# Optimization experiments

Measured on AMD Instinct MI355X. Metric: run time of the kernel, lower is better.

## Reference

```python
import jax, jax.numpy as jnp
import numpy as np
from jax import lax

EPS = 1e-5
B, NA, NE, NAL = 1024, 10, 10, 9

def qbn(x):
    # QBN_RM1d: divide by RMS of detached input over all dims but last
    xd = lax.stop_gradient(x)
    mean2 = jnp.mean((xd * xd).reshape(-1, xd.shape[-1]), axis=0)
    return x / jnpp_sqrt(mean2) if False else x / jnp.sqrt(mean2 + EPS)

def qrelu(x):
    # Qrelu1d: scale each 2-vector (axis -2) by mod/max(1,mod), mod from detached x
    xd = lax.stop_gradient(x)
    mod = jnp.sqrt(jnp.sum(xd * xd, axis=-2))
    coeff = mod / jnp.maximum(1.0, mod)
    return x * coeff[..., None, :]

def rcn(x, Ws):
    for W in Ws:
        x = qrelu(qbn(x @ W))
    return x

def qmerge(x):
    return jnp.sum(x * x, axis=-2)

def qmaxpool(x):
    # x: [B,A,N,2,C]; pick per-channel entity with max squared 2-norm
    xd = lax.stop_gradient(x)
    mod = jnp.sum(xd * xd, axis=-2)            # [B,A,N,C]
    idx = jnp.argmax(mod, axis=-2)             # [B,A,C]
    idxb = jnp.broadcast_to(idx[:, :, None, None, :], x.shape[:2] + (1,) + x.shape[-2:])
    return jnp.take_along_axis(x, idxb, axis=-3)[:, :, 0]   # [B,A,2,C]

def build_vec(feats, own_vec):
    # feats: [B,A,n,9]; own_vec: [B,A,2,11]
    pos = feats[..., 2:4][..., None]                          # [B,A,n,2,1]
    pos_mod = jnp.sqrt(jnp.sum(pos * pos, axis=-2))           # [B,A,n,1]
    other = jnp.concatenate([feats[..., :2], feats[..., 4:]], axis=-1)  # [B,A,n,7]
    other_mod = jnp.sqrt(2.0 * other * other)                 # repeat-2 then 2-norm = sqrt(2*x^2)
    mask = pos_mod == 0.0
    denom = jnp.where(mask, 1.0, pos_mod)
    coff = jnp.where(mask, 0.0, other_mod / denom)[..., None, :]   # [B,A,n,1,7]
    vec = pos * coff                                           # [B,A,n,2,7]
    own_mod = jnp.sqrt(jnp.sum(own_vec * own_vec, axis=-2))[:, :, None, :]  # [B,A,1,11]
    own_coff = jnp.where(mask, 0.0, own_mod / denom)[..., None, :]          # [B,A,n,1,11]
    own_vecf = pos * own_coff                                  # [B,A,n,2,11]
    return jnp.concatenate([pos, vec, own_vecf], axis=-1)      # [B,A,n,2,19]

def setup_inputs() -> dict:
    key = jax.random.key(0)
    ks = jax.random.split(key, 32)
    s = 0.1
    inp = {
        'own_feats':   jax.random.normal(ks[0], (B, NA, 11), jnp.float32),
        'enemy_feats': jax.random.normal(ks[1], (B, NA, NE, 9), jnp.float32),
        'ally_feats':  jax.random.normal(ks[2], (B, NA, NAL, 9), jnp.float32),
        'W_e1': jax.random.normal(ks[3], (19, 64), jnp.float32) * s,
        'W_e2': jax.random.normal(ks[4], (64, 64), jnp.float32) * s,
        'W_a1': jax.random.normal(ks[5], (19, 64), jnp.float32) * s,
        'W_a2': jax.random.normal(ks[6], (64, 64), jnp.float32) * s,
        'W_f1': jax.random.normal(ks[7], (64, 64), jnp.float32) * s,
        'W_f2': jax.random.normal(ks[8], (64, 64), jnp.float32) * s,
        'W_ie1': jax.random.normal(ks[9], (128, 64), jnp.float32) * s,
        'W_ie2': jax.random.normal(ks[10], (64, 64), jnp.float32) * s,
        'W_ie3': jax.random.normal(ks[11], (64, 1), jnp.float32) * s,
        'W_ia1': jax.random.normal(ks[12], (128, 64), jnp.float32) * s,
        'W_ia2': jax.random.normal(ks[13], (64, 64), jnp.float32) * s,
        'W_ia3': jax.random.normal(ks[14], (64, 1), jnp.float32) * s,
        'W_oa1': jax.random.normal(ks[15], (64, 64), jnp.float32) * s,
        'b_oa1': jnp.zeros((64,), jnp.float32),
        'W_oa2': jax.random.normal(ks[16], (64, 3), jnp.float32) * s,
        'b_oa2': jnp.zeros((3,), jnp.float32),
        'W_at1': jax.random.normal(ks[17], (128, 128), jnp.float32) * s,
        'b_at1': jnp.zeros((128,), jnp.float32),
        'W_at2': jax.random.normal(ks[18], (128, 64), jnp.float32) * s,
        'b_at2': jnp.zeros((64,), jnp.float32),
        'W_at3': jax.random.normal(ks[19], (64, 1), jnp.float32) * s,
        'b_at3': jnp.zeros((1,), jnp.float32),
    }
    return inp

def reference(own_feats, enemy_feats, ally_feats,
              W_e1, W_e2, W_a1, W_a2, W_f1, W_f2,
              W_ie1, W_ie2, W_ie3, W_ia1, W_ia2, W_ia3,
              W_oa1, b_oa1, W_oa2, b_oa2,
              W_at1, b_at1, W_at2, b_at2, W_at3, b_at3):
    Bc = own_feats.shape[0]
    own_vec = jnp.repeat(own_feats[:, :, None, :], 2, axis=2)        # [B,A,2,11]
    ev = build_vec(enemy_feats, own_vec)                              # [B,A,10,2,19]
    av = build_vec(ally_feats, own_vec)                               # [B,A,9,2,19]
    e_rc = rcn(ev, (W_e1, W_e2))                                      # [B,A,10,2,64]
    e_scalar = qmerge(e_rc)                                           # [B,A,10,64]
    a_rc = rcn(av, (W_a1, W_a2))                                      # [B,A,9,2,64]
    all_rc = jnp.concatenate([e_rc, a_rc], axis=-3)                   # [B,A,19,2,64]
    vf = rcn(qmaxpool(all_rc), (W_f1, W_f2))                          # [B,A,2,64]
    vrep = jnp.broadcast_to(vf[:, :, None], (Bc, NA, NE, 2, 64))
    cat = jnp.concatenate([vrep, e_rc], axis=-1)                      # [B,A,10,2,128]
    e_imp = rcn(cat, (W_ie1, W_ie2, W_ie3))                           # [B,A,10,2,1]
    a_imp = rcn(cat, (W_ia1, W_ia2, W_ia3))                           # (orig code also uses enemy feats here)
    move_vec = jnp.sum(jnp.concatenate([e_imp, a_imp], axis=-3), axis=-3)  # [B,A,2,1]
    sf = qmerge(vf)                                                   # [B,A,64]
    oaq = jax.nn.relu(sf @ W_oa1 + b_oa1) @ W_oa2 + b_oa2             # [B,A,3]
    mmq = oaq[:, :, 2:3]
    up = mmq + move_vec[:, :, 1, :]
    down = mmq - move_vec[:, :, 1, :]
    right = mmq + move_vec[:, :, 0, :]
    left = mmq - move_vec[:, :, 0, :]
    move_q = jnp.concatenate([up, down, right, left], axis=-1)        # [B,A,4]
    sfr = jnp.broadcast_to(sf[:, :, None, :], (Bc, NA, NE, 64))
    atf = jnp.concatenate([sfr, e_scalar], axis=-1)                   # [B,A,10,128]
    h = jax.nn.relu(atf @ W_at1 + b_at1)
    h = jax.nn.relu(h @ W_at2 + b_at2)
    aq = (h @ W_at3 + b_at3)[..., 0]                                  # [B,A,10]
    return jnp.concatenate([oaq[:, :, 0:2], move_q, aq], axis=-1)     # [B,A,16]
```

## Files before the change

### kernel.cpp

```cpp
#include <hip/hip_runtime.h>
#include <math.h>

#define BATCH 1024
#define NA 10
#define NEN 10
#define NALY 9
#define NAG (BATCH*NA)
#define NEE (NAG*NEN)
#define NAE (NAG*NALY)
#define EPSF 1e-5f

#define DOFF_SE1 0
#define DOFF_SE2 1024
#define DOFF_SA1 2048
#define DOFF_SA2 3072
#define DOFF_SF1 4096
#define DOFF_SF2 5120
#define DOFF_SIE1 6144
#define DOFF_SIE2 7168
#define DOFF_SIA1 8192
#define DOFF_SIA2 9216
#define DOFF_SIE3 10240
#define DOFF_SIA3 10368
#define NDOUBLES 16384

#define NBLK_BE (NEE/8)
#define NBLK_BA (NAE/8)
#define NBLK_PE64 (NEE/64)
#define NBLK_PA64 (NAE/64)

__device__ __forceinline__ double sum16vd(const double* __restrict__ S, int ch) {
    double s = 0.0;
#pragma unroll
    for (int r = 0; r < 16; ++r) s += S[r*64 + ch];
    return s;
}
__device__ __forceinline__ double sum16sd8(const double* __restrict__ S) {
    double s = 0.0;
#pragma unroll
    for (int r = 0; r < 16; ++r) s += S[r*8];
    return s;
}
__device__ __forceinline__ float qbn_s(const double* __restrict__ S, int ch, double invRows) {
    float m = (float)(sum16vd(S, ch)*invRows);
    return sqrtf(m + EPSF);
}
__device__ __forceinline__ void red_to_S(const double* red, double* S, int bid, int tid) {
    if (tid < 64) {
        double v = red[tid] + red[tid+64] + red[tid+128] + red[tid+192];
        atomicAdd(&S[(bid & 15)*64 + tid], v);
    }
}
__device__ __forceinline__ float pair_m2(float x0, float x1) {
    return __fadd_rn(__fmul_rn(x0,x0), __fmul_rn(x1,x1));
}
__device__ __forceinline__ float qcoef(float mod) {
    return fminf(mod, 1.0f);
}

__global__ __launch_bounds__(256) void k_build_both(
    const float* __restrict__ ef, const float* __restrict__ af,
    const float* __restrict__ own,
    const float* __restrict__ We1, const float* __restrict__ Wa1,
    float* __restrict__ XE, float* __restrict__ XA,
    double* __restrict__ SE1, double* __restrict__ SA1)
{
    bool isA = (blockIdx.x >= NBLK_BE);
    int blk = isA ? (blockIdx.x - NBLK_BE) : blockIdx.x;
    const float* feats = isA ? af : ef;
    const float* W1    = isA ? Wa1 : We1;
    float* X           = isA ? XA : XE;
    double* S1         = isA ? SA1 : SE1;
    int nEntPerAgent   = isA ? NALY : NEN;

    __shared__ float wlds[19*64];
    __shared__ float gpc[16][19];
    __shared__ double red[256];
    int tid = threadIdx.x;
    for (int i = tid; i < 19*64; i += 256) wlds[i] = W1[i];
    if (tid < 152) {
        int el = tid / 19, chg = tid % 19;
        int ent = blk*8 + el;
        const float* f = feats + (size_t)ent*9;
        int agent = ent / nEntPerAgent;
        float px = f[2], py = f[3];
        float pm = sqrtf(__fadd_rn(__fmul_rn(px,px), __fmul_rn(py,py)));
        float val;
        if (chg == 0) val = 1.f;
        else if (chg < 8) {
            int j = chg - 1;
            int fi = (j < 2) ? j : (j + 2);
            float o = f[fi];
            float om = sqrtf(__fmul_rn(__fmul_rn(2.0f,o),o));
            val = (pm == 0.f) ? 0.f : __fdiv_rn(om, pm);
        } else {
            float o = own[(size_t)agent*11 + (chg-8)];
            float t = __fmul_rn(o,o);
            float om = sqrtf(__fadd_rn(t,t));
            val = (pm == 0.f) ? 0.f : __fdiv_rn(om, pm);
        }
        gpc[el*2 + 0][chg] = __fmul_rn(px, val);
        gpc[el*2 + 1][chg] = __fmul_rn(py, val);
    }
    __syncthreads();
    int l = tid >> 7, c = (tid >> 6) & 1, ch = tid & 63;
    float wreg[19];
#pragma unroll
    for (int k = 0; k < 19; ++k) wreg[k] = wlds[k*64+ch];
    double lr = 0.0;
#pragma unroll
    for (int i = 0; i < 4; ++i) {
        int el = l + 2*i;
        int ent = blk*8 + el;
        int row = el*2 + c;
        float acc = 0.f;
#pragma unroll
        for (int k = 18; k >= 0; --k) {
            acc = fmaf(gpc[row][k], wreg[k], acc);
        }
        X[(size_t)ent*128 + c*64 + ch] = acc;
        lr += (double)acc * (double)acc;
    }
    red[tid] = lr;
    __syncthreads();
    red_to_S(red, S1, blk, tid);
}

__device__ __forceinline__ void pair_layer_body(
    float* __restrict__ X, const double* __restrict__ Sin, double* __restrict__ Sout,
    const float* __restrict__ W, double invRows, int blk)
{
    __shared__ float wlds[4096];
    __shared__ __align__(16) float ybuf[64][132];
    __shared__ float ss[64];
    double* dredw = (double*)&ybuf[0][0];
    int tid = threadIdx.x;
    for (int i = tid; i < 4096; i += 512) wlds[i] = W[i];
    if (tid < 64) ss[tid] = qbn_s(Sin, tid, invRows);
    __syncthreads();
    int rl = tid >> 4;
    int ch0 = (tid & 15) * 4;
#pragma unroll
    for (int h = 0; h < 2; ++h) {
        int r = rl + h*32;
        size_t row = (size_t)blk*64 + r;
        float4 xv0 = *(const float4*)&X[row*128 + ch0];
        float4 xv1 = *(const float4*)&X[row*128 + 64 + ch0];
        float xs0[4] = {xv0.x,xv0.y,xv0.z,xv0.w};
        float xs1[4] = {xv1.x,xv1.y,xv1.z,xv1.w};
        float y0[4], y1[4];
#pragma unroll
        for (int i = 0; i < 4; ++i) {
            float s = ss[ch0+i];
            float u0 = xs0[i]/s, u1 = xs1[i]/s;
            float mod = sqrtf(pair_m2(u0,u1));
            float cf = qcoef(mod);
            y0[i] = __fmul_rn(u0,cf);
            y1[i] = __fmul_rn(u1,cf);
        }
        *(float4*)&ybuf[r][2*ch0]     = make_float4(y0[0],y1[0],y0[1],y1[1]);
        *(float4*)&ybuf[r][2*ch0 + 4] = make_float4(y0[2],y1[2],y0[3],y1[3]);
    }
    __syncthreads();
    float a0[4] = {0.f,0.f,0.f,0.f};
    float a1[4] = {0.f,0.f,0.f,0.f};
    float c0[4] = {0.f,0.f,0.f,0.f};
    float c1[4] = {0.f,0.f,0.f,0.f};
#pragma unroll
    for (int k = 63; k >= 1; k -= 2) {
        float4 wk  = *(const float4*)&wlds[k*64 + ch0];
        float4 wk1 = *(const float4*)&wlds[(k-1)*64 + ch0];
        float4 ya  = *(const float4*)&ybuf[rl][2*k - 2];
        float4 yb  = *(const float4*)&ybuf[rl+32][2*k - 2];
        float wkv[4]  = {wk.x,wk.y,wk.z,wk.w};
        float wk1v[4] = {wk1.x,wk1.y,wk1.z,wk1.w};
#pragma unroll
        for (int i = 0; i < 4; ++i) {
            a0[i] = fmaf(ya.z, wkv[i], a0[i]);
            a1[i] = fmaf(ya.w, wkv[i], a1[i]);
        }
#pragma unroll
        for (int i = 0; i < 4; ++i) {
            a0[i] = fmaf(ya.x, wk1v[i], a0[i]);
            a1[i] = fmaf(ya.y, wk1v[i], a1[i]);
        }
#pragma unroll
        for (int i = 0; i < 4; ++i) {
            c0[i] = fmaf(yb.z, wkv[i], c0[i]);
            c1[i] = fmaf(yb.w, wkv[i], c1[i]);
        }
#pragma unroll
        for (int i = 0; i < 4; ++i) {
            c0[i] = fmaf(yb.x, wk1v[i], c0[i]);
            c1[i] = fmaf(yb.y, wk1v[i], c1[i]);
        }
    }
    size_t rowA = (size_t)blk*64 + rl;
    size_t rowB = rowA + 32;
    *(float4*)&X[rowA*128 + ch0]      = make_float4(a0[0],a0[1],a0[2],a0[3]);
    *(float4*)&X[rowA*128 + 64 + ch0] = make_float4(a1[0],a1[1],a1[2],a1[3]);
    *(float4*)&X[rowB*128 + ch0]      = make_float4(c0[0],c0[1],c0[2],c0[3]);
    *(float4*)&X[rowB*128 + 64 + ch0] = make_float4(c1[0],c1[1],c1[2],c1[3]);
    __syncthreads();
    {
        int wv = tid >> 6;
#pragma unroll
        for (int i = 0; i < 4; ++i) {
            double d = (double)a0[i]*a0[i] + (double)a1[i]*a1[i]
                     + (double)c0[i]*c0[i] + (double)c1[i]*c1[i];
            d += __shfl_xor(d, 16, 64);
            d += __shfl_xor(d, 32, 64);
            if ((tid & 48) == 0) dredw[wv*64 + ch0+i] = d;
        }
    }
    __syncthreads();
    if (tid < 64) {
        double v = 0.0;
#pragma unroll
        for (int w = 0; w < 8; ++w) v += dredw[w*64 + tid];
        atomicAdd(&Sout[(blk & 15)*64 + tid], v);
    }
}

__global__ __launch_bounds__(512) void k_pair_both(
    float* __restrict__ XE, const double* __restrict__ SE1, double* __restrict__ SE2,
    const float* __restrict__ We2, double invRe,
    float* __restrict__ XA, const double* __restrict__ SA1, double* __restrict__ SA2,
    const float* __restrict__ Wa2, double invRa)
{
    if (blockIdx.x < NBLK_PE64)
        pair_layer_body(XE, SE1, SE2, We2, invRe, blockIdx.x);
    else
        pair_layer_body(XA, SA1, SA2, Wa2, invRa, blockIdx.x - NBLK_PE64);
}

__global__ __launch_bounds__(512) void k_pair_layer(
    float* __restrict__ X, const double* __restrict__ Sin, double* __restrict__ Sout,
    const float* __restrict__ W, double invRows)
{
    pair_layer_body(X, Sin, Sout, W, invRows, blockIdx.x);
}

__global__ __launch_bounds__(256) void k_finalize_pair(
    float* __restrict__ X, const double* __restrict__ S2, double invRows,
    float* __restrict__ ESC)
{
    __shared__ float ss[64];
    if (threadIdx.x < 64) ss[threadIdx.x] = qbn_s(S2, threadIdx.x, invRows);
    int t = blockIdx.x*256 + threadIdx.x;
    int rl = t >> 4;
    int ch0 = (t & 15) * 4;
    size_t base    = (size_t)rl*64 + ch0;
    size_t partner = (size_t)(rl ^ 1)*64 + ch0;
    float4 xv  = *(const float4*)&X[base];
    float4 xov = *(const float4*)&X[partner];
    __syncthreads();
    float xs[4]  = {xv.x,xv.y,xv.z,xv.w};
    float xos[4] = {xov.x,xov.y,xov.z,xov.w};
    float r[4], esc[4];
    int c = rl & 1;
#pragma unroll
    for (int i = 0; i < 4; ++i) {
        float s = ss[ch0+i];
        float u  = xs[i]/s;
        float uo = xos[i]/s;
        float u0 = (c==0) ? u : uo, u1 = (c==0) ? uo : u;
        float mod = sqrtf(pair_m2(u0,u1));
        float cf = qcoef(mod);
        r[i] = __fmul_rn(u, cf);
        if (c == 0) {
            float y1v = __fmul_rn(uo, cf);
            esc[i] = pair_m2(r[i], y1v);
        }
    }
    *(float4*)&X[base] = make_float4(r[0],r[1],r[2],r[3]);
    if (c == 0) {
        int ent = rl >> 1;
        *(float4*)&ESC[(size_t)ent*64 + ch0] = make_float4(esc[0],esc[1],esc[2],esc[3]);
    }
}

__global__ __launch_bounds__(256) void k_pool_f1(
    const float* __restrict__ XE, const float* __restrict__ XAraw,
    const double* __restrict__ SA2, double invRa,
    const float* __restrict__ Wf1, float* __restrict__ F1, double* __restrict__ Sf1)
{
    __shared__ float wlds[4096];
    __shared__ float v[4][2][64];
    __shared__ float ssa[64];
    __shared__ double red[256];
    int tid = threadIdx.x;
    for (int i = tid; i < 4096; i += 256) wlds[i] = Wf1[i];
    if (tid < 64) ssa[tid] = qbn_s(SA2, tid, invRa);
    __syncthreads();
    int grp = tid>>6, ch = tid&63;
    int agent = blockIdx.x*4 + grp;
    float best = -1.f, v0 = 0.f, v1 = 0.f;
    for (int e = 0; e < NEN; ++e) {
        size_t b = (size_t)(agent*NEN+e)*128;
        float x0 = XE[b+ch], x1 = XE[b+64+ch];
        float m2 = pair_m2(x0,x1);
        if (m2 > best) { best = m2; v0 = x0; v1 = x1; }
    }
    float sa = ssa[ch];
    for (int l = 0; l < NALY; ++l) {
        size_t b = (size_t)(agent*NALY+l)*128;
        float r0 = XAraw[b+ch], r1 = XAraw[b+64+ch];
        float u0 = r0/sa, u1 = r1/sa;
        float modf = sqrtf(pair_m2(u0,u1));
        float cff = qcoef(modf);
        float x0 = __fmul_rn(u0,cff), x1 = __fmul_rn(u1,cff);
        float m2 = pair_m2(x0,x1);
        if (m2 > best) { best = m2; v0 = x0; v1 = x1; }
    }
    v[grp][0][ch] = v0; v[grp][1][ch] = v1;
    __syncthreads();
    float a0 = 0.f, a1 = 0.f;
#pragma unroll
    for (int k = 0; k < 64; ++k) {
        float w = wlds[k*64+ch];
        a0 = fmaf(v[grp][0][k], w, a0);
        a1 = fmaf(v[grp][1][k], w, a1);
    }
    F1[(size_t)agent*128+ch] = a0; F1[(size_t)agent*128+64+ch] = a1;
    red[tid] = (double)a0*a0 + (double)a1*a1;
    __syncthreads();
    red_to_S(red, Sf1, blockIdx.x, tid);
}

__global__ __launch_bounds__(256) void k_vf_vtop(
    float* __restrict__ F1, const double* __restrict__ Sf2,
    float* __restrict__ SFb,
    const float* __restrict__ Wie1, const float* __restrict__ Wia1,
    const float* __restrict__ Wat1, const float* __restrict__ bat1,
    float* __restrict__ VTie, float* __restrict__ VTia, double invRows)
{
    __shared__ float wie[4096];
    __shared__ float wia[4096];
    __shared__ float vf[4][2][64];
    __shared__ float sfv[4][64];
    int tid = threadIdx.x;
    for (int i = tid; i < 4096; i += 256) { wie[i] = Wie1[i]; wia[i] = Wia1[i]; }
    int grp = tid>>6, ch = tid&63;
    int agent = blockIdx.x*4 + grp;
    float x0 = F1[(size_t)agent*128+ch], x1 = F1[(size_t)agent*128+64+ch];
    float s = qbn_s(Sf2, ch, invRows);
    float u0 = x0/s, u1 = x1/s;
    float mod = sqrtf(pair_m2(u0,u1));
    float cf = qcoef(mod);
    float y0 = __fmul_rn(u0,cf), y1 = __fmul_rn(u1,cf);
    vf[grp][0][ch] = y0; vf[grp][1][ch] = y1;
    float sf = pair_m2(y0,y1);
    SFb[(size_t)agent*64+ch] = sf;
    sfv[grp][ch] = sf;
    __syncthreads();
    float a0=0.f,a1=0.f,b0=0.f,b1=0.f;
    float at0 = bat1[ch], at1 = bat1[64+ch];
#pragma unroll
    for (int k = 0; k < 64; ++k) {
        float f0 = vf[grp][0][k], f1 = vf[grp][1][k];
        a0 = fmaf(f0, wie[k*64+ch], a0); a1 = fmaf(f1, wie[k*64+ch], a1);
        b0 = fmaf(f0, wia[k*64+ch], b0); b1 = fmaf(f1, wia[k*64+ch], b1);
        float sv = sfv[grp][k];
        at0 = fmaf(sv, Wat1[k*128 + ch], at0);
        at1 = fmaf(sv, Wat1[k*128 + 64 + ch], at1);
    }
    VTie[(size_t)agent*128+ch] = a0; VTie[(size_t)agent*128+64+ch] = a1;
    VTia[(size_t)agent*128+ch] = b0; VTia[(size_t)agent*128+64+ch] = b1;
    F1[(size_t)agent*128+ch] = at0; F1[(size_t)agent*128+64+ch] = at1;
}

__global__ __launch_bounds__(512) void k_imp1_both(
    float* __restrict__ XE,
    const float* __restrict__ VTe, const float* __restrict__ VTa,
    const float* __restrict__ W1e, const float* __restrict__ W1a,
    float* __restrict__ XIe,
    double* __restrict__ S1e, double* __restrict__ S1a)
{
    __shared__ float wldsE[4096];
    __shared__ float wldsA[4096];
    __shared__ __align__(16) float xt[64][68];
    double* dredwE = (double*)&xt[0][0];
    double* dredwA = dredwE + 512;
    int tid = threadIdx.x;
    for (int i = tid; i < 4096; i += 512) { wldsE[i] = W1e[4096 + i]; wldsA[i] = W1a[4096 + i]; }
#pragma unroll
    for (int i = 0; i < 2; ++i) {
        int fidx = tid + i*512;
        int r = fidx >> 4;
        int kq = (fidx & 15) * 4;
        float4 t4 = *(const float4*)&XE[(size_t)blockIdx.x*4096 + (size_t)fidx*4];
        *(float4*)&xt[r][kq] = t4;
    }
    __syncthreads();
    int rl = tid >> 4;
    int ch0 = (tid & 15) * 4;
    int entA = blockIdx.x*32 + (rl >> 1);
    int entB = entA + 16;
    int c = rl & 1;
    int agentA = entA / NEN, agentB = entB / NEN;
    float4 vteA = *(const float4*)&VTe[(size_t)agentA*128 + c*64 + ch0];
    float4 vtaA = *(const float4*)&VTa[(size_t)agentA*128 + c*64 + ch0];
    float4 vteB = *(const float4*)&VTe[(size_t)agentB*128 + c*64 + ch0];
    float4 vtaB = *(const float4*)&VTa[(size_t)agentB*128 + c*64 + ch0];
    float accEA[4] = {vteA.x, vteA.y, vteA.z, vteA.w};
    float accAA[4] = {vtaA.x, vtaA.y, vtaA.z, vtaA.w};
    float accEB[4] = {vteB.x, vteB.y, vteB.z, vteB.w};
    float accAB[4] = {vtaB.x, vtaB.y, vtaB.z, vtaB.w};
#pragma unroll
    for (int k = 0; k < 64; k += 4) {
        float4 xa4 = *(const float4*)&xt[rl][k];
        float4 xb4 = *(const float4*)&xt[rl+32][k];
        float xa[4] = {xa4.x, xa4.y, xa4.z, xa4.w};
        float xb[4] = {xb4.x, xb4.y, xb4.z, xb4.w};
#pragma unroll
        for (int kk = 0; kk < 4; ++kk) {
            float4 we = *(const float4*)&wldsE[(k+kk)*64 + ch0];
            accEA[0] = fmaf(xa[kk], we.x, accEA[0]);
            accEA[1] = fmaf(xa[kk], we.y, accEA[1]);
            accEA[2] = fmaf(xa[kk], we.z, accEA[2]);
            accEA[3] = fmaf(xa[kk], we.w, accEA[3]);
            accEB[0] = fmaf(xb[kk], we.x, accEB[0]);
            accEB[1] = fmaf(xb[kk], we.y, accEB[1]);
            accEB[2] = fmaf(xb[kk], we.z, accEB[2]);
            accEB[3] = fmaf(xb[kk], we.w, accEB[3]);
            float4 wa = *(const float4*)&wldsA[(k+kk)*64 + ch0];
            accAA[0] = fmaf(xa[kk], wa.x, accAA[0]);
            accAA[1] = fmaf(xa[kk], wa.y, accAA[1]);
            accAA[2] = fmaf(xa[kk], wa.z, accAA[2]);
            accAA[3] = fmaf(xa[kk], wa.w, accAA[3]);
            accAB[0] = fmaf(xb[kk], wa.x, accAB[0]);
            accAB[1] = fmaf(xb[kk], wa.y, accAB[1]);
            accAB[2] = fmaf(xb[kk], wa.z, accAB[2]);
            accAB[3] = fmaf(xb[kk], wa.w, accAB[3]);
        }
    }
    *(float4*)&XIe[(size_t)entA*128 + c*64 + ch0] = make_float4(accEA[0],accEA[1],accEA[2],accEA[3]);
    *(float4*)&XIe[(size_t)entB*128 + c*64 + ch0] = make_float4(accEB[0],accEB[1],accEB[2],accEB[3]);
    *(float4*)&XE [(size_t)entA*128 + c*64 + ch0] = make_float4(accAA[0],accAA[1],accAA[2],accAA[3]);
    *(float4*)&XE [(size_t)entB*128 + c*64 + ch0] = make_float4(accAB[0],accAB[1],accAB[2],accAB[3]);
    __syncthreads();
    int wv = tid >> 6;
#pragma unroll
    for (int i = 0; i < 4; ++i) {
        double dE = (double)accEA[i]*accEA[i] + (double)accEB[i]*accEB[i];
        dE += __shfl_xor(dE, 16, 64);
        dE += __shfl_xor(dE, 32, 64);
        double dA = (double)accAA[i]*accAA[i] + (double)accAB[i]*accAB[i];
        dA += __shfl_xor(dA, 16, 64);
        dA += __shfl_xor(dA, 32, 64);
        if ((tid & 48) == 0) {
            dredwE[wv*64 + ch0+i] = dE;
            dredwA[wv*64 + ch0+i] = dA;
        }
    }
    __syncthreads();
    if (tid < 64) {
        double vE = 0.0, vA = 0.0;
#pragma unroll
        for (int w = 0; w < 8; ++w) { vE += dredwE[w*64 + tid]; vA += dredwA[w*64 + tid]; }
        atomicAdd(&S1e[(blockIdx.x & 15)*64 + tid], vE);
        atomicAdd(&S1a[(blockIdx.x & 15)*64 + tid], vA);
    }
}

__global__ __launch_bounds__(256) void k_imp3_both(
    const float* __restrict__ XIe, const float* __restrict__ XIa,
    const double* __restrict__ S2e, const double* __restrict__ S2a,
    const float* __restrict__ W3e, const float* __restrict__ W3a,
    float* __restrict__ Ze, float* __restrict__ Za,
    double* __restrict__ S3e, double* __restrict__ S3a, double invRows)
{
    bool isA = (blockIdx.x >= (NEE/16));
    int blk = isA ? (blockIdx.x - NEE/16) : blockIdx.x;
    const float* XI = isA ? XIa : XIe;
    const double* S2 = isA ? S2a : S2e;
    const float* W3 = isA ? W3a : W3e;
    float* Z = isA ? Za : Ze;
    double* S3 = isA ? S3a : S3e;

    __shared__ float ss[64];
    __shared__ double red4[4];
    int tid = threadIdx.x; int grp = tid>>6, ch = tid&63;
    if (tid < 64) ss[tid] = qbn_s(S2, tid, invRows);
    __syncthreads();
    float s = ss[ch];
    double w3 = (double)W3[ch];
    double lr3 = 0.0;
#pragma unroll
    for (int i = 0; i < 4; ++i) {
        int ent = blk*16 + grp + 4*i;
        float x0 = XI[(size_t)ent*128+ch], x1 = XI[(size_t)ent*128+64+ch];
        float u0 = x0/s, u1 = x1/s;
        float mod = sqrtf(pair_m2(u0,u1));
        float cf = qcoef(mod);
        double v0 = (double)__fmul_rn(u0,cf) * w3;
        double v1 = (double)__fmul_rn(u1,cf) * w3;
#pragma unroll
        for (int m = 1; m < 64; m <<= 1) { v0 += __shfl_xor(v0,m,64); v1 += __shfl_xor(v1,m,64); }
        if (ch == 0) {
            float z0 = (float)v0, z1 = (float)v1;
            Z[(size_t)ent*2] = z0; Z[(size_t)ent*2+1] = z1;
            lr3 += (double)z0*z0 + (double)z1*z1;
        }
    }
    if (ch == 0) red4[grp] = lr3;
    __syncthreads();
    if (tid == 0) atomicAdd(&S3[(blk & 15)*8], red4[0]+red4[1]+red4[2]+red4[3]);
}

__global__ __launch_bounds__(256) void k_final_small(
    const float* __restrict__ Zie, const float* __restrict__ Zia,
    const double* __restrict__ Sie3, const double* __restrict__ Sia3,
    const float* __restrict__ SFb,
    const float* __restrict__ Woa1, const float* __restrict__ boa1,
    const float* __restrict__ Woa2, const float* __restrict__ boa2,
    float* __restrict__ out, double invRows)
{
    __shared__ float sflds[4][64];
    int tid = threadIdx.x; int grp = tid>>6, ch = tid&63;
    int agent = blockIdx.x*4 + grp;
    float sie = sqrtf((float)(sum16sd8(Sie3)*invRows) + EPSF);
    float sia = sqrtf((float)(sum16sd8(Sia3)*invRows) + EPSF);
    double pv0 = 0.0, pv1 = 0.0;
    if (ch < NEN) {
        int ent = agent*NEN + ch;
        float z0 = Zie[(size_t)ent*2]/sie, z1 = Zie[(size_t)ent*2+1]/sie;
        float mod = sqrtf(pair_m2(z0,z1)); float cf = qcoef(mod);
        pv0 = (double)__fmul_rn(z0,cf); pv1 = (double)__fmul_rn(z1,cf);
        z0 = Zia[(size_t)ent*2]/sia; z1 = Zia[(size_t)ent*2+1]/sia;
        mod = sqrtf(pair_m2(z0,z1)); cf = qcoef(mod);
        pv0 += (double)__fmul_rn(z0,cf); pv1 += (double)__fmul_rn(z1,cf);
    }
#pragma unroll
    for (int m = 1; m < 64; m <<= 1) { pv0 += __shfl_xor(pv0,m,64); pv1 += __shfl_xor(pv1,m,64); }
    sflds[grp][ch] = SFb[(size_t)agent*64+ch];
    __syncthreads();
    double hd = (double)boa1[ch];
#pragma unroll
    for (int k = 0; k < 64; ++k) hd += (double)sflds[grp][k]*(double)Woa1[k*64+ch];
    float h = fmaxf((float)hd, 0.f);
    double q0 = (double)h*(double)Woa2[ch*3+0];
    double q1 = (double)h*(double)Woa2[ch*3+1];
    double q2 = (double)h*(double)Woa2[ch*3+2];
#pragma unroll
    for (int m = 1; m < 64; m <<= 1) { q0 += __shfl_xor(q0,m,64); q1 += __shfl_xor(q1,m,64); q2 += __shfl_xor(q2,m,64); }
    if (ch == 0) {
        float oaq0 = (float)(q0 + (double)boa2[0]);
        float oaq1 = (float)(q1 + (double)boa2[1]);
        float mmq  = (float)(q2 + (double)boa2[2]);
        float mv0 = (float)pv0, mv1 = (float)pv1;
        float* o = out + (size_t)agent*16;
        o[0] = oaq0; o[1] = oaq1;
        o[2] = mmq + mv1; o[3] = mmq - mv1;
        o[4] = mmq + mv0; o[5] = mmq - mv0;
    }
}

__global__ __launch_bounds__(256) void k_attn(
    const float* __restrict__ ATtop, const float* __restrict__ ESC,
    const float* __restrict__ W1,
    const float* __restrict__ W2, const float* __restrict__ b2,
    const float* __restrict__ W3, const float* __restrict__ b3,
    float* __restrict__ out)
{
    __shared__ float escT[64][20];
    __shared__ float h1T[128][20];
    __shared__ float h2[16][68];
    int tid = threadIdx.x;
    int row0 = blockIdx.x*16;
#pragma unroll
    for (int i = 0; i < 4; ++i) {
        int idx = tid + i*256; int r = idx>>6; int j = idx&63;
        escT[j][r] = ESC[(size_t)(row0 + r)*64 + j];
    }
    __syncthreads();
    {
        int j = tid & 127, rr = tid >> 7;
        float acc[8];
#pragma unroll
        for (int r = 0; r < 8; ++r) {
            int ent = row0 + rr*8 + r; int agent = ent/NEN;
            acc[r] = ATtop[(size_t)agent*128 + j];
        }
#pragma unroll 8
        for (int k = 0; k < 64; ++k) {
            float w = W1[(64 + k)*128 + j];
            float4 a0 = *(const float4*)&escT[k][rr*8];
            float4 a1 = *(const float4*)&escT[k][rr*8 + 4];
            acc[0] = fmaf(a0.x, w, acc[0]);
            acc[1] = fmaf(a0.y, w, acc[1]);
            acc[2] = fmaf(a0.z, w, acc[2]);
            acc[3] = fmaf(a0.w, w, acc[3]);
            acc[4] = fmaf(a1.x, w, acc[4]);
            acc[5] = fmaf(a1.y, w, acc[5]);
            acc[6] = fmaf(a1.z, w, acc[6]);
            acc[7] = fmaf(a1.w, w, acc[7]);
        }
        float4 o0 = make_float4(fmaxf(acc[0],0.f), fmaxf(acc[1],0.f),
                                fmaxf(acc[2],0.f), fmaxf(acc[3],0.f));
        float4 o1 = make_float4(fmaxf(acc[4],0.f), fmaxf(acc[5],0.f),
                                fmaxf(acc[6],0.f), fmaxf(acc[7],0.f));
        *(float4*)&h1T[j][rr*8]     = o0;
        *(float4*)&h1T[j][rr*8 + 4] = o1;
    }
    __syncthreads();
    {
        int j2 = tid & 63, rr2 = tid >> 6;
        float bb = b2[j2];
        float acc[4] = {bb, bb, bb, bb};
#pragma unroll 8
        for (int k = 0; k < 128; ++k) {
            float w = W2[k*64 + j2];
            float4 p = *(const float4*)&h1T[k][rr2*4];
            acc[0] = fmaf(p.x, w, acc[0]);
            acc[1] = fmaf(p.y, w, acc[1]);
            acc[2] = fmaf(p.z, w, acc[2]);
            acc[3] = fmaf(p.w, w, acc[3]);
        }
#pragma unroll
        for (int r = 0; r < 4; ++r) h2[rr2*4+r][j2] = fmaxf(acc[r], 0.f);
    }
    __syncthreads();
    {
        int r3 = tid >> 4, l3 = tid & 15;
        float s = 0.f;
#pragma unroll
        for (int q = 0; q < 4; ++q) s = fmaf(h2[r3][l3 + 16*q], W3[l3 + 16*q], s);
#pragma unroll
        for (int m = 1; m < 16; m <<= 1) s += __shfl_xor(s, m, 64);
        if (l3 == 0) {
            int ent = row0 + r3; int agent = ent/NEN; int e = ent%NEN;
            out[(size_t)agent*16 + 6 + e] = s + b3[0];
        }
    }
}

extern "C" void kernel_launch(void* const* d_in, const int* in_sizes, int n_in,
                              void* d_out, int out_size, void* d_ws, size_t ws_size,
                              hipStream_t stream) {
    const float* own  = (const float*)d_in[0];
    const float* ef   = (const float*)d_in[1];
    const float* af   = (const float*)d_in[2];
    const float* W_e1 = (const float*)d_in[3];
    const float* W_e2 = (const float*)d_in[4];
    const float* W_a1 = (const float*)d_in[5];
    const float* W_a2 = (const float*)d_in[6];
    const float* W_f1 = (const float*)d_in[7];
    const float* W_f2 = (const float*)d_in[8];
    const float* W_ie1= (const float*)d_in[9];
    const float* W_ie2= (const float*)d_in[10];
    const float* W_ie3= (const float*)d_in[11];
    const float* W_ia1= (const float*)d_in[12];
    const float* W_ia2= (const float*)d_in[13];
    const float* W_ia3= (const float*)d_in[14];
    const float* W_oa1= (const float*)d_in[15];
    const float* b_oa1= (const float*)d_in[16];
    const float* W_oa2= (const float*)d_in[17];
    const float* b_oa2= (const float*)d_in[18];
    const float* W_at1= (const float*)d_in[19];
    const float* b_at1= (const float*)d_in[20];
    const float* W_at2= (const float*)d_in[21];
    const float* b_at2= (const float*)d_in[22];
    const float* W_at3= (const float*)d_in[23];
    const float* b_at3= (const float*)d_in[24];
    float* out = (float*)d_out;
    float* wsf = (float*)d_ws;
    double* Sd = (double*)d_ws;

    size_t o = (size_t)NDOUBLES*2;
    float*  X_E  = wsf + o; o += (size_t)NEE*128;
    float*  X_A  = wsf + o; o += (size_t)NAE*128;
    float*  F1   = wsf + o; o += (size_t)NAG*128;
    float*  SFb  = wsf + o; o += (size_t)NAG*64;
    float*  VT_IE = wsf + o; o += (size_t)NAG*128;
    float*  VT_IA = wsf + o; o += (size_t)NAG*128;
    float*  XI   = wsf + o; o += (size_t)NEE*128;
    float*  Z_IE = wsf + o; o += (size_t)NEE*2;
    float*  Z_IA = wsf + o; o += (size_t)NEE*2;
    float*  ESC  = wsf + o; o += (size_t)NEE*64;

    double* S_E1 = Sd + DOFF_SE1;  double* S_E2 = Sd + DOFF_SE2;
    double* S_A1 = Sd + DOFF_SA1;  double* S_A2 = Sd + DOFF_SA2;
    double* S_F1 = Sd + DOFF_SF1;  double* S_F2 = Sd + DOFF_SF2;
    double* S_IE1= Sd + DOFF_SIE1; double* S_IE2= Sd + DOFF_SIE2;
    double* S_IA1= Sd + DOFF_SIA1; double* S_IA2= Sd + DOFF_SIA2;
    double* S_IE3= Sd + DOFF_SIE3; double* S_IA3= Sd + DOFF_SIA3;

    const double invRe = 1.0/(double)(NEE*2);
    const double invRa = 1.0/(double)(NAE*2);
    const double invRf = 1.0/(double)(NAG*2);

    hipMemsetAsync(Sd, 0, (size_t)NDOUBLES*sizeof(double), stream);

    k_build_both<<<NBLK_BE + NBLK_BA, 256, 0, stream>>>(
        ef, af, own, W_e1, W_a1, X_E, X_A, S_E1, S_A1);
    k_pair_both<<<NBLK_PE64 + NBLK_PA64, 512, 0, stream>>>(
        X_E, S_E1, S_E2, W_e2, invRe, X_A, S_A1, S_A2, W_a2, invRa);
    k_finalize_pair<<<NEE*32/256, 256, 0, stream>>>(X_E, S_E2, invRe, ESC);
    k_pool_f1<<<NAG/4, 256, 0, stream>>>(X_E, X_A, S_A2, invRa, W_f1, F1, S_F1);
    k_pair_layer<<<NAG/64, 512, 0, stream>>>(F1, S_F1, S_F2, W_f2, invRf);
    k_vf_vtop<<<NAG/4, 256, 0, stream>>>(F1, S_F2, SFb, W_ie1, W_ia1,
                                         W_at1, b_at1, VT_IE, VT_IA, invRf);
    k_imp1_both<<<NEE/32, 512, 0, stream>>>(X_E, VT_IE, VT_IA, W_ie1, W_ia1,
                                            XI, S_IE1, S_IA1);
    k_pair_both<<<NBLK_PE64 + NBLK_PE64, 512, 0, stream>>>(
        XI, S_IE1, S_IE2, W_ie2, invRe, X_E, S_IA1, S_IA2, W_ia2, invRe);
    k_imp3_both<<<2*(NEE/16), 256, 0, stream>>>(XI, X_E, S_IE2, S_IA2,
                                                W_ie3, W_ia3, Z_IE, Z_IA,
                                                S_IE3, S_IA3, invRe);

    k_final_small<<<NAG/4, 256, 0, stream>>>(Z_IE, Z_IA, S_IE3, S_IA3, SFb,
                                             W_oa1, b_oa1, W_oa2, b_oa2, out, invRe);
    k_attn<<<NEE/16, 256, 0, stream>>>(F1, ESC, W_at1, W_at2, b_at2,
                                       W_at3, b_at3, out);
}
```

Baseline: 551.3 us.

## Register-tile attention MLP over 32 rows per block with vectorized weight loads

```diff
diff --git a/kernel.cpp b/kernel.cpp
--- a/kernel.cpp
+++ b/kernel.cpp
@@ -564,74 +564,87 @@
     const float* __restrict__ W3, const float* __restrict__ b3,
     float* __restrict__ out)
 {
-    __shared__ float escT[64][20];
-    __shared__ float h1T[128][20];
-    __shared__ float h2[16][68];
+    __shared__ __align__(16) float escT[64][36];
+    __shared__ __align__(16) float h1T[128][36];
+    float (*h2)[68] = (float(*)[68])&escT[0][0];
     int tid = threadIdx.x;
-    int row0 = blockIdx.x*16;
-#pragma unroll
-    for (int i = 0; i < 4; ++i) {
+    int row0 = blockIdx.x*32;
+#pragma unroll
+    for (int i = 0; i < 8; ++i) {
         int idx = tid + i*256; int r = idx>>6; int j = idx&63;
         escT[j][r] = ESC[(size_t)(row0 + r)*64 + j];
     }
     __syncthreads();
     {
-        int j = tid & 127, rr = tid >> 7;
-        float acc[8];
-#pragma unroll
-        for (int r = 0; r < 8; ++r) {
-            int ent = row0 + rr*8 + r; int agent = ent/NEN;
-            acc[r] = ATtop[(size_t)agent*128 + j];
-        }
-#pragma unroll 8
+        int j0 = (tid & 31)*4;
+        int rr = tid >> 5;
+        float acc[4][4];
+#pragma unroll
+        for (int ri = 0; ri < 4; ++ri) {
+            int ent = row0 + rr*4 + ri; int agent = ent/NEN;
+            float4 t = *(const float4*)&ATtop[(size_t)agent*128 + j0];
+            acc[0][ri]=t.x; acc[1][ri]=t.y; acc[2][ri]=t.z; acc[3][ri]=t.w;
+        }
+#pragma unroll 4
         for (int k = 0; k < 64; ++k) {
-            float w = W1[(64 + k)*128 + j];
-            float4 a0 = *(const float4*)&escT[k][rr*8];
-            float4 a1 = *(const float4*)&escT[k][rr*8 + 4];
-            acc[0] = fmaf(a0.x, w, acc[0]);
-            acc[1] = fmaf(a0.y, w, acc[1]);
-            acc[2] = fmaf(a0.z, w, acc[2]);
-            acc[3] = fmaf(a0.w, w, acc[3]);
-            acc[4] = fmaf(a1.x, w, acc[4]);
-            acc[5] = fmaf(a1.y, w, acc[5]);
-            acc[6] = fmaf(a1.z, w, acc[6]);
-            acc[7] = fmaf(a1.w, w, acc[7]);
-        }
-        float4 o0 = make_float4(fmaxf(acc[0],0.f), fmaxf(acc[1],0.f),
-                                fmaxf(acc[2],0.f), fmaxf(acc[3],0.f));
-        float4 o1 = make_float4(fmaxf(acc[4],0.f), fmaxf(acc[5],0.f),
-                                fmaxf(acc[6],0.f), fmaxf(acc[7],0.f));
-        *(float4*)&h1T[j][rr*8]     = o0;
-        *(float4*)&h1T[j][rr*8 + 4] = o1;
+            float4 w = *(const float4*)&W1[(size_t)(64+k)*128 + j0];
+            float4 e = *(const float4*)&escT[k][rr*4];
+            float wv[4] = {w.x,w.y,w.z,w.w};
+            float ev[4] = {e.x,e.y,e.z,e.w};
+#pragma unroll
+            for (int ji = 0; ji < 4; ++ji)
+#pragma unroll
+                for (int ri = 0; ri < 4; ++ri)
+                    acc[ji][ri] = fmaf(ev[ri], wv[ji], acc[ji][ri]);
+        }
+#pragma unroll
+        for (int ji = 0; ji < 4; ++ji) {
+            float4 o = make_float4(fmaxf(acc[ji][0],0.f), fmaxf(acc[ji][1],0.f),
+                                   fmaxf(acc[ji][2],0.f), fmaxf(acc[ji][3],0.f));
+            *(float4*)&h1T[j0+ji][rr*4] = o;
+        }
     }
     __syncthreads();
     {
-        int j2 = tid & 63, rr2 = tid >> 6;
-        float bb = b2[j2];
-        float acc[4] = {bb, bb, bb, bb};
+        int j20 = (tid & 15)*4;
+        int rr2 = tid >> 4;
+        float acc[4][2];
+#pragma unroll
+        for (int ji = 0; ji < 4; ++ji) {
+            float bb = b2[j20+ji];
+            acc[ji][0] = bb; acc[ji][1] = bb;
+        }
 #pragma unroll 8
         for (int k = 0; k < 128; ++k) {
-            float w = W2[k*64 + j2];
-            float4 p = *(const float4*)&h1T[k][rr2*4];
-            acc[0] = fmaf(p.x, w, acc[0]);
-            acc[1] = fmaf(p.y, w, acc[1]);
-            acc[2] = fmaf(p.z, w, acc[2]);
-            acc[3] = fmaf(p.w, w, acc[3]);
-        }
-#pragma unroll
-        for (int r = 0; r < 4; ++r) h2[rr2*4+r][j2] = fmaxf(acc[r], 0.f);
+            float4 w = *(const float4*)&W2[(size_t)k*64 + j20];
+            float2 p = *(const float2*)&h1T[k][rr2*2];
+            float wv[4] = {w.x,w.y,w.z,w.w};
+#pragma unroll
+            for (int ji = 0; ji < 4; ++ji) {
+                acc[ji][0] = fmaf(p.x, wv[ji], acc[ji][0]);
+                acc[ji][1] = fmaf(p.y, wv[ji], acc[ji][1]);
+            }
+        }
+#pragma unroll
+        for (int ji = 0; ji < 4; ++ji) {
+            h2[rr2*2+0][j20+ji] = fmaxf(acc[ji][0], 0.f);
+            h2[rr2*2+1][j20+ji] = fmaxf(acc[ji][1], 0.f);
+        }
     }
     __syncthreads();
     {
-        int r3 = tid >> 4, l3 = tid & 15;
-        float s = 0.f;
-#pragma unroll
-        for (int q = 0; q < 4; ++q) s = fmaf(h2[r3][l3 + 16*q], W3[l3 + 16*q], s);
-#pragma unroll
-        for (int m = 1; m < 16; m <<= 1) s += __shfl_xor(s, m, 64);
-        if (l3 == 0) {
-            int ent = row0 + r3; int agent = ent/NEN; int e = ent%NEN;
-            out[(size_t)agent*16 + 6 + e] = s + b3[0];
+#pragma unroll
+        for (int half = 0; half < 2; ++half) {
+            int r3 = (tid >> 4) + half*16, l3 = tid & 15;
+            float s = 0.f;
+#pragma unroll
+            for (int q = 0; q < 4; ++q) s = fmaf(h2[r3][l3 + 16*q], W3[l3 + 16*q], s);
+#pragma unroll
+            for (int m = 1; m < 16; m <<= 1) s += __shfl_xor(s, m, 64);
+            if (l3 == 0) {
+                int ent = row0 + r3; int agent = ent/NEN; int e = ent%NEN;
+                out[(size_t)agent*16 + 6 + e] = s + b3[0];
+            }
         }
     }
 }
@@ -712,6 +725,6 @@
 
     k_final_small<<<NAG/4, 256, 0, stream>>>(Z_IE, Z_IA, S_IE3, S_IA3, SFb,
                                              W_oa1, b_oa1, W_oa2, b_oa2, out, invRe);
-    k_attn<<<NEE/16, 256, 0, stream>>>(F1, ESC, W_at1, W_at2, b_at2,
+    k_attn<<<NEE/32, 256, 0, stream>>>(F1, ESC, W_at1, W_at2, b_at2,
                                        W_at3, b_at3, out);
 }
```

Measured after the change: 591.6 us. 7.3% more time.
